# Kernel tuning notes

Hardware: AMD Instinct MI355X
Metric: run time of the kernel (lower is better)

The kernel has to match this reference:

```python
import jax, jax.numpy as jnp
import numpy as np
from jax import lax

H = 256        # hidden_size
T = 576        # history length (PERIOD*24)
F_T = 24       # future steps
M = 32         # m_features
B = 256        # batch
PERIOD = T // 24
E = 2 * H      # encoder output dim (bidirectional)
EPS = 1e-6     # torch PairwiseDistance eps


def setup_inputs() -> dict:
    key = jax.random.key(0)
    ks = jax.random.split(key, 16)
    rn = lambda k, sh, s=1.0: jax.random.normal(k, sh, jnp.float32) * s
    return {
        "input_encoded": rn(ks[0], (B, T, E)),
        "feature_history1": rn(ks[1], (B, T, M)),
        "y_history": rn(ks[2], (B, T, 1)),               # unused by forward (matches torch)
        "feature_future1": rn(ks[3], (B, F_T, M)),
        "hidden": rn(ks[4], (2, B, H), 0.1),
        "cell": rn(ks[5], (2, B, H), 0.1),
        # attn_layer: Linear(2H+M -> T), Tanh, Linear(T -> T)
        "attn_W1": rn(ks[6], (T, E + M), 0.05), "attn_b1": jnp.zeros((T,), jnp.float32),
        "attn_W2": rn(ks[7], (T, T), 0.05),     "attn_b2": jnp.zeros((T,), jnp.float32),
        # bidirectional 1-layer LSTM, stacked over direction d in {fwd, bwd}
        "W_ih": rn(ks[8], (2, 4 * H, E + M), 0.05),
        "W_hh": rn(ks[9], (2, 4 * H, H), 0.05),
        "b_ih": jnp.zeros((2, 4 * H), jnp.float32),
        "b_hh": jnp.zeros((2, 4 * H), jnp.float32),
        # fc_final: Linear(2H -> H), ReLU, Linear(H -> 1)
        "fcf_W1": rn(ks[10], (H, E), 0.05), "fcf_b1": jnp.zeros((H,), jnp.float32),
        "fcf_W2": rn(ks[11], (1, H), 0.05), "fcf_b2": jnp.zeros((1,), jnp.float32),
    }


def reference(input_encoded, feature_history1, y_history, feature_future1,
              hidden, cell, attn_W1, attn_b1, attn_W2, attn_b2,
              W_ih, W_hh, b_ih, b_hh, fcf_W1, fcf_b1, fcf_W2, fcf_b2):
    b = input_encoded.shape[0]
    # --- period-similarity weights alpha (computed once) ---
    fh = feature_history1.reshape(b, PERIOD, 24, M)                 # [B,period,24,M]
    # pairwise L2 distance between future [B,24,1,M] and history hours [B,24,period,M]
    diff = feature_future1[:, :, None, :] - fh.transpose(0, 2, 1, 3)  # [B,24,period,M]
    dist = jnp.sqrt(jnp.sum((diff + EPS) ** 2, axis=-1))            # [B,24,period]
    dp = 1.0 / jnp.sum(dist, axis=2)                                # rsqrt(.)**2 == 1/x; [B,24]
    alpha = jax.nn.softmax(dp, axis=1)                              # [B,24] (period==24)
    enc = input_encoded.reshape(b, PERIOD, 24, E)                   # [B,period,24,E]
    bias = (b_ih + b_hh)[:, None, :]                                # [2,1,4H]

    def step(carry, ff_t):                                          # ff_t: [B,M]
        h, c = carry                                                # each [2,B,H]
        x = jnp.concatenate([h[0], h[1], ff_t], axis=1)             # [B,2H+M]
        a = jnp.tanh(x @ attn_W1.T + attn_b1) @ attn_W2.T + attn_b2
        a = jax.nn.softmax(a, axis=1)                               # [B,T]
        w = a.reshape(b, PERIOD, 24)                                # [B,period,24]
        # context: sum attention-weighted encodings over each day, then alpha over periods
        ctx = jnp.einsum('bpk,bpke,bp->be', w, enc, alpha)          # [B,E]
        inp = jnp.concatenate([ctx, ff_t], axis=1)                  # [B,2H+M]
        gates = (jnp.einsum('bi,dgi->dbg', inp, W_ih)
                 + jnp.einsum('dbh,dgh->dbg', h, W_hh) + bias)      # [2,B,4H]
        i_g, f_g, g_g, o_g = jnp.split(gates, 4, axis=-1)           # torch gate order i,f,g,o
        c_new = jax.nn.sigmoid(f_g) * c + jax.nn.sigmoid(i_g) * jnp.tanh(g_g)
        h_new = jax.nn.sigmoid(o_g) * jnp.tanh(c_new)               # [2,B,H]
        hh = jnp.concatenate([h_new[0], h_new[1]], axis=1)          # [B,2H]
        y = jax.nn.relu(hh @ fcf_W1.T + fcf_b1) @ fcf_W2.T + fcf_b2  # [B,1]
        return (h_new, c_new), y

    _, ys = lax.scan(step, (hidden, cell), jnp.transpose(feature_future1, (1, 0, 2)))
    return jnp.transpose(ys, (1, 0, 2))                             # [B,f_T,1]
```

## Files before the change

kernel.cpp:

```cpp
#include <hip/hip_runtime.h>
#include <math.h>

#define B_ 256
#define T_ 576
#define FT_ 24
#define M_ 32
#define H_ 256
#define E_ 512
#define KX_ 544
#define ND_ 2048
#define EPS_ 1e-6f
#define LDAS 72

typedef __attribute__((ext_vector_type(8))) short bf8;
typedef __attribute__((ext_vector_type(4))) float f4;

__device__ __forceinline__ float bf2f(unsigned short s) {
    union { unsigned u; float f; } c; c.u = ((unsigned)s) << 16; return c.f;
}
__device__ __forceinline__ short f2bf(float f) {
    union { float f; unsigned u; } c; c.f = f;
    unsigned r = c.u + 0x7fffu + ((c.u >> 16) & 1u);
    return (short)(r >> 16);
}
__device__ __forceinline__ float sigm(float x) { return 1.f / (1.f + expf(-x)); }

__device__ __forceinline__ void mfma4(const short (*As)[LDAS], const short (*Bs)[LDAS],
                                      int wm, int wn, int fr, int fk, f4 acc[2][2]) {
    bf8 a0 = *(const bf8*)&As[wm + fr][fk];
    bf8 a1 = *(const bf8*)&As[wm + 16 + fr][fk];
    bf8 b0 = *(const bf8*)&Bs[wn + fr][fk];
    bf8 b1 = *(const bf8*)&Bs[wn + 16 + fr][fk];
    acc[0][0] = __builtin_amdgcn_mfma_f32_16x16x32_bf16(a0, b0, acc[0][0], 0, 0, 0);
    acc[0][1] = __builtin_amdgcn_mfma_f32_16x16x32_bf16(a0, b1, acc[0][1], 0, 0, 0);
    acc[1][0] = __builtin_amdgcn_mfma_f32_16x16x32_bf16(a1, b0, acc[1][0], 0, 0, 0);
    acc[1][1] = __builtin_amdgcn_mfma_f32_16x16x32_bf16(a1, b1, acc[1][1], 0, 0, 0);
}

__device__ __forceinline__ void gemm64(const short* __restrict__ A, int lda,
                                       const short* __restrict__ Wt, int ldw, int K,
                                       short (*As)[LDAS], short (*Bs)[LDAS], int tid,
                                       f4 acc[2][2]) {
    int lane = tid & 63, w = tid >> 6;
    int wm = (w & 1) * 32, wn = (w >> 1) * 32;
    int fr = lane & 15, fk = (lane >> 4) * 8;
    int r = tid >> 2, c0 = (tid & 3) * 16, c8 = (tid & 3) * 8;
    int4 pa0, pa1, pb0, pb1;
    auto ld = [&](int k0) {
        if (K - k0 >= 64) {
            pa0 = *(const int4*)(A + r * lda + k0 + c0);
            pa1 = *(const int4*)(A + r * lda + k0 + c0 + 8);
            pb0 = *(const int4*)(Wt + r * ldw + k0 + c0);
            pb1 = *(const int4*)(Wt + r * ldw + k0 + c0 + 8);
        } else {
            pa0 = *(const int4*)(A + r * lda + k0 + c8);
            pb0 = *(const int4*)(Wt + r * ldw + k0 + c8);
        }
    };
    ld(0);
    for (int k0 = 0; k0 < K; k0 += 64) {
        int rem = K - k0;
        if (rem >= 64) {
            *(int4*)&As[r][c0] = pa0; *(int4*)&As[r][c0 + 8] = pa1;
            *(int4*)&Bs[r][c0] = pb0; *(int4*)&Bs[r][c0 + 8] = pb1;
        } else {
            *(int4*)&As[r][c8] = pa0;
            *(int4*)&Bs[r][c8] = pb0;
        }
        __syncthreads();
        if (k0 + 64 < K) ld(k0 + 64);
        mfma4(As, Bs, wm, wn, fr, fk, acc);
        if (rem >= 64) mfma4(As, Bs, wm, wn, fr, fk + 32, acc);
        __syncthreads();
    }
}

struct SetupPrm {
    const float *enc, *fhist, *ff, *hidden, *cell;
    const float *aW1, *aW2, *Wih, *Whh, *bih, *bhh, *fW1;
    short *W1b, *W2b, *Wihb, *Whhb, *fW1b, *encb, *xb, *hA;
    float *bcomb, *alpha, *cbuf;
};

__global__ __launch_bounds__(256) void k_setup(SetupPrm p) {
    const int NT = 2048 * 256;
    int gt = blockIdx.x * 256 + threadIdx.x;
    auto cast = [&](const float* s, short* d, int n4) {
        for (int i = gt; i < n4; i += NT) {
            float4 v = ((const float4*)s)[i];
            short4 o; o.x = f2bf(v.x); o.y = f2bf(v.y); o.z = f2bf(v.z); o.w = f2bf(v.w);
            ((short4*)d)[i] = o;
        }
    };
    cast(p.aW1, p.W1b, T_ * KX_ / 4);
    cast(p.aW2, p.W2b, T_ * T_ / 4);
    cast(p.fW1, p.fW1b, H_ * E_ / 4);
    cast(p.enc, p.encb, B_ * T_ * E_ / 4);
    for (int i = gt; i < ND_ * KX_ / 4; i += NT) {
        int row = i / (KX_ / 4), c4 = i % (KX_ / 4);
        int d = row >> 10, rest = row & 1023, j = rest >> 2, g = rest & 3;
        int orig = d * 1024 + g * 256 + j;
        float4 v = ((const float4*)(p.Wih + orig * KX_))[c4];
        short4 o; o.x = f2bf(v.x); o.y = f2bf(v.y); o.z = f2bf(v.z); o.w = f2bf(v.w);
        ((short4*)(p.Wihb + row * KX_))[c4] = o;
    }
    for (int i = gt; i < ND_ * H_ / 4; i += NT) {
        int row = i / (H_ / 4), c4 = i % (H_ / 4);
        int d = row >> 10, rest = row & 1023, j = rest >> 2, g = rest & 3;
        int orig = d * 1024 + g * 256 + j;
        float4 v = ((const float4*)(p.Whh + orig * H_))[c4];
        short4 o; o.x = f2bf(v.x); o.y = f2bf(v.y); o.z = f2bf(v.z); o.w = f2bf(v.w);
        ((short4*)(p.Whhb + row * H_))[c4] = o;
    }
    for (int i = gt; i < ND_; i += NT) {
        int d = i >> 10, rest = i & 1023, j = rest >> 2, g = rest & 3;
        int orig = d * 1024 + g * 256 + j;
        p.bcomb[i] = p.bih[orig] + p.bhh[orig];
    }
    for (int i = gt; i < 2 * B_ * H_; i += NT) {
        int d = i >> 16, b = (i >> 8) & 255, j = i & 255;
        short hv = f2bf(p.hidden[i]);
        p.xb[b * KX_ + d * H_ + j] = hv;
        p.hA[i] = hv;
        p.cbuf[i] = p.cell[i];
        if (d == 0 && j < M_) p.xb[b * KX_ + E_ + j] = f2bf(p.ff[b * FT_ * M_ + j]);
    }
    if (blockIdx.x < 256 && threadIdx.x < 64) {
        int b = blockIdx.x, t = threadIdx.x;
        float dp = 0.f;
        if (t < 24) {
            float fv[M_];
            const float* fp = p.ff + (b * FT_ + t) * M_;
            #pragma unroll
            for (int m = 0; m < M_; m++) fv[m] = fp[m];
            float dist = 0.f;
            for (int pp = 0; pp < 24; pp++) {
                const float* hp = p.fhist + (b * T_ + pp * 24 + t) * M_;
                float s = 0.f;
                #pragma unroll
                for (int m = 0; m < M_; m++) { float d = fv[m] - hp[m] + EPS_; s += d * d; }
                dist += sqrtf(s);
            }
            dp = 1.f / dist;
        }
        float v = (t < 24) ? dp : -INFINITY;
        float mx = v;
        for (int off = 32; off; off >>= 1) mx = fmaxf(mx, __shfl_xor(mx, off));
        float e = (t < 24) ? expf(dp - mx) : 0.f;
        float sme = e;
        for (int off = 32; off; off >>= 1) sme += __shfl_xor(sme, off);
        if (t < 24) p.alpha[b * 24 + t] = e / sme;
    }
}

__global__ __launch_bounds__(256) void k_a1fc(const short* __restrict__ xb,
                                              const short* __restrict__ W1b,
                                              const float* __restrict__ ab1,
                                              short* __restrict__ s1,
                                              const short* __restrict__ fW1b,
                                              const float* __restrict__ fb1,
                                              const float* __restrict__ fW2,
                                              float* __restrict__ out, int t) {
    __shared__ short As[64][LDAS];
    __shared__ short Bs[64][LDAS];
    __shared__ float ypart[64];
    int tid = threadIdx.x;
    int lane = tid & 63, w = tid >> 6;
    int wm = (w & 1) * 32, wn = (w >> 1) * 32;
    int m0 = blockIdx.y * 64;
    if (blockIdx.x < 9) {
        int n0 = blockIdx.x * 64;
        f4 acc[2][2] = {};
        gemm64(xb + m0 * KX_, KX_, W1b + n0 * KX_, KX_, KX_, As, Bs, tid, acc);
        int colb = n0 + wn + (lane & 15);
        int rowb = m0 + wm + (lane >> 4) * 4;
        #pragma unroll
        for (int im = 0; im < 2; im++)
            #pragma unroll
            for (int in = 0; in < 2; in++) {
                int col = colb + in * 16;
                float bv = ab1[col];
                #pragma unroll
                for (int q = 0; q < 4; q++)
                    s1[(rowb + im * 16 + q) * T_ + col] = f2bf(tanhf(acc[im][in][q] + bv));
            }
    } else {
        if (t == 0) return;
        int step = t - 1;
        int n0 = (blockIdx.x - 9) * 64;
        f4 acc[2][2] = {};
        gemm64(xb + m0 * KX_, KX_, fW1b + n0 * E_, E_, E_, As, Bs, tid, acc);
        if (tid < 64) ypart[tid] = 0.f;
        __syncthreads();
        int colb = n0 + wn + (lane & 15);
        int rloc = wm + (lane >> 4) * 4;
        #pragma unroll
        for (int im = 0; im < 2; im++)
            #pragma unroll
            for (int q = 0; q < 4; q++) {
                float s = 0.f;
                #pragma unroll
                for (int in = 0; in < 2; in++) {
                    int col = colb + in * 16;
                    s += fmaxf(acc[im][in][q] + fb1[col], 0.f) * fW2[col];
                }
                #pragma unroll
                for (int off = 1; off < 16; off <<= 1) s += __shfl_xor(s, off);
                if ((lane & 15) == 0) atomicAdd(&ypart[rloc + im * 16 + q], s);
            }
        __syncthreads();
        if (tid < 64) atomicAdd(&out[(m0 + tid) * FT_ + step], ypart[tid]);
    }
}

__global__ __launch_bounds__(256) void k_a2(const short* __restrict__ s1,
                                            const short* __restrict__ W2b,
                                            const float* __restrict__ ab2,
                                            float* __restrict__ logit) {
    __shared__ short As[64][LDAS];
    __shared__ short Bs[64][LDAS];
    int n0 = blockIdx.x * 64, m0 = blockIdx.y * 64, tid = threadIdx.x;
    f4 acc[2][2] = {};
    gemm64(s1 + m0 * T_, T_, W2b + n0 * T_, T_, T_, As, Bs, tid, acc);
    int lane = tid & 63, w = tid >> 6;
    int wm = (w & 1) * 32, wn = (w >> 1) * 32;
    int colb = n0 + wn + (lane & 15);
    int rowb = m0 + wm + (lane >> 4) * 4;
    #pragma unroll
    for (int im = 0; im < 2; im++)
        #pragma unroll
        for (int in = 0; in < 2; in++) {
            int col = colb + in * 16;
            float bv = ab2[col];
            #pragma unroll
            for (int q = 0; q < 4; q++)
                logit[(rowb + im * 16 + q) * T_ + col] = acc[im][in][q] + bv;
        }
}

__global__ __launch_bounds__(256) void k_ctx(const float* __restrict__ logits,
                                             const float* __restrict__ alpha,
                                             const short* __restrict__ encb,
                                             float* __restrict__ ctx) {
    int b = blockIdx.x >> 3, s = blockIdx.x & 7;
    int tid = threadIdx.x;
    __shared__ float wt[T_];
    __shared__ float red4[4];
    __shared__ float red[8][64];
    const float* lg = logits + b * T_;
    float l0 = lg[tid], l1 = lg[tid + 256];
    float l2 = (tid < 64) ? lg[tid + 512] : -INFINITY;
    float mx = fmaxf(fmaxf(l0, l1), l2);
    for (int off = 32; off; off >>= 1) mx = fmaxf(mx, __shfl_xor(mx, off));
    if ((tid & 63) == 0) red4[tid >> 6] = mx;
    __syncthreads();
    mx = fmaxf(fmaxf(red4[0], red4[1]), fmaxf(red4[2], red4[3]));
    float e0 = expf(l0 - mx), e1 = expf(l1 - mx);
    float e2 = (tid < 64) ? expf(l2 - mx) : 0.f;
    float sme = e0 + e1 + e2;
    for (int off = 32; off; off >>= 1) sme += __shfl_xor(sme, off);
    __syncthreads();
    if ((tid & 63) == 0) red4[tid >> 6] = sme;
    __syncthreads();
    float inv = 1.f / (red4[0] + red4[1] + red4[2] + red4[3]);
    const float* al = alpha + b * 24;
    wt[tid]       = e0 * inv * al[tid / 24];
    wt[tid + 256] = e1 * inv * al[(tid + 256) / 24];
    if (tid < 64) wt[tid + 512] = e2 * inv * al[(tid + 512) / 24];
    __syncthreads();
    int chp = tid & 31, rg = tid >> 5;
    int c0 = s * 64;
    float a0 = 0.f, a1 = 0.f;
    const unsigned* ep = (const unsigned*)(encb + ((size_t)b * T_ + rg * 72) * E_ + c0) + chp;
    const float* wl = wt + rg * 72;
    #pragma unroll 8
    for (int it = 0; it < 72; it++) {
        float wv = wl[it];
        unsigned u = ep[(size_t)it * (E_ / 2)];
        a0 += wv * bf2f((unsigned short)(u & 0xffffu));
        a1 += wv * bf2f((unsigned short)(u >> 16));
    }
    *(float2*)&red[rg][chp * 2] = make_float2(a0, a1);
    __syncthreads();
    if (tid < 64) {
        float sum = 0.f;
        #pragma unroll
        for (int r = 0; r < 8; r++) sum += red[r][tid];
        ctx[b * E_ + c0 + tid] = sum;
    }
}

__global__ __launch_bounds__(256) void k_gl(const float* __restrict__ ctxp,
                                            const float* __restrict__ ff, int t,
                                            short* __restrict__ xb,
                                            const short* __restrict__ Wihb,
                                            const short* __restrict__ Whhb,
                                            const float* __restrict__ bcomb,
                                            float* __restrict__ cbuf,
                                            const short* __restrict__ hprev,
                                            short* __restrict__ hnext,
                                            const float* __restrict__ fb2,
                                            float* __restrict__ out) {
    __shared__ union {
        struct { short As[64][LDAS]; short Bs[64][LDAS]; } g;
        float gt[64][68];
    } sm;
    int n0 = blockIdx.x * 64, m0 = blockIdx.y * 64, tid = threadIdx.x;
    int lane = tid & 63, w = tid >> 6;
    int wm = (w & 1) * 32, wn = (w >> 1) * 32;
    int fr = lane & 15, fk = (lane >> 4) * 8;
    int r = tid >> 2, c0 = (tid & 3) * 16, c8 = (tid & 3) * 8;
    f4 acc[2][2] = {};
    for (int k0 = 0; k0 < KX_; k0 += 64) {
        int rem = KX_ - k0;
        if (rem >= 64) {
            const float* cp = ctxp + (m0 + r) * E_ + k0 + c0;
            short av[16];
            #pragma unroll
            for (int i = 0; i < 16; i++) av[i] = f2bf(cp[i]);
            *(int4*)&sm.g.As[r][c0]     = *(int4*)&av[0];
            *(int4*)&sm.g.As[r][c0 + 8] = *(int4*)&av[8];
            *(int4*)&sm.g.Bs[r][c0]     = *(const int4*)(Wihb + (n0 + r) * KX_ + k0 + c0);
            *(int4*)&sm.g.Bs[r][c0 + 8] = *(const int4*)(Wihb + (n0 + r) * KX_ + k0 + c0 + 8);
        } else {
            const float* fp = ff + ((m0 + r) * FT_ + t) * M_ + (k0 + c8 - E_);
            short av[8];
            #pragma unroll
            for (int i = 0; i < 8; i++) av[i] = f2bf(fp[i]);
            *(int4*)&sm.g.As[r][c8] = *(int4*)&av[0];
            *(int4*)&sm.g.Bs[r][c8] = *(const int4*)(Wihb + (n0 + r) * KX_ + k0 + c8);
        }
        __syncthreads();
        mfma4(sm.g.As, sm.g.Bs, wm, wn, fr, fk, acc);
        if (rem >= 64) mfma4(sm.g.As, sm.g.Bs, wm, wn, fr, fk + 32, acc);
        __syncthreads();
    }
    int d = n0 >> 10;
    gemm64(hprev + d * B_ * H_ + m0 * H_, H_, Whhb + n0 * H_, H_, H_,
           sm.g.As, sm.g.Bs, tid, acc);
    int clb = wn + (lane & 15);
    int rlb = wm + (lane >> 4) * 4;
    #pragma unroll
    for (int im = 0; im < 2; im++)
        #pragma unroll
        for (int in = 0; in < 2; in++) {
            int cl = clb + in * 16;
            float bv = bcomb[n0 + cl];
            #pragma unroll
            for (int q = 0; q < 4; q++)
                sm.gt[rlb + im * 16 + q][cl] = acc[im][in][q] + bv;
        }
    __syncthreads();
    int j0 = (n0 >> 2) & 255;
    #pragma unroll
    for (int it = 0; it < 4; it++) {
        int item = tid + it * 256;
        int rl = item >> 4, ql = item & 15;
        float ig = sm.gt[rl][ql * 4 + 0];
        float fg = sm.gt[rl][ql * 4 + 1];
        float gg = sm.gt[rl][ql * 4 + 2];
        float og = sm.gt[rl][ql * 4 + 3];
        int b = m0 + rl, j = j0 + ql;
        int ci = d * 65536 + b * 256 + j;
        float cn = sigm(fg) * cbuf[ci] + sigm(ig) * tanhf(gg);
        float hn = sigm(og) * tanhf(cn);
        cbuf[ci] = cn;
        short hv = f2bf(hn);
        xb[b * KX_ + d * H_ + j] = hv;
        hnext[ci] = hv;
        if (d == 0 && j < M_ && t + 1 < FT_)
            xb[b * KX_ + E_ + j] = f2bf(ff[(b * FT_ + t + 1) * M_ + j]);
        if (n0 == 0 && ql == 0) out[b * FT_ + t] = fb2[0];
    }
}

__global__ __launch_bounds__(256) void k_fc(const short* __restrict__ xb,
                                            const short* __restrict__ fW1b,
                                            const float* __restrict__ fb1,
                                            const float* __restrict__ fW2,
                                            float* __restrict__ out, int step) {
    __shared__ short As[64][LDAS];
    __shared__ short Bs[64][LDAS];
    __shared__ float ypart[64];
    int fb = blockIdx.x, tid = threadIdx.x;
    int m0 = (fb >> 2) * 64, n0 = (fb & 3) * 64;
    f4 acc[2][2] = {};
    gemm64(xb + m0 * KX_, KX_, fW1b + n0 * E_, E_, E_, As, Bs, tid, acc);
    if (tid < 64) ypart[tid] = 0.f;
    __syncthreads();
    int lane = tid & 63, w = tid >> 6;
    int wm = (w & 1) * 32, wn = (w >> 1) * 32;
    int colb = n0 + wn + (lane & 15);
    int rloc = wm + (lane >> 4) * 4;
    #pragma unroll
    for (int im = 0; im < 2; im++)
        #pragma unroll
        for (int q = 0; q < 4; q++) {
            float s = 0.f;
            #pragma unroll
            for (int in = 0; in < 2; in++) {
                int col = colb + in * 16;
                s += fmaxf(acc[im][in][q] + fb1[col], 0.f) * fW2[col];
            }
            #pragma unroll
            for (int off = 1; off < 16; off <<= 1) s += __shfl_xor(s, off);
            if ((lane & 15) == 0) atomicAdd(&ypart[rloc + im * 16 + q], s);
        }
    __syncthreads();
    if (tid < 64) atomicAdd(&out[(m0 + tid) * FT_ + step], ypart[tid]);
}

extern "C" void kernel_launch(void* const* d_in, const int* in_sizes, int n_in,
                              void* d_out, int out_size, void* d_ws, size_t ws_size,
                              hipStream_t stream) {
    (void)in_sizes; (void)n_in; (void)out_size; (void)ws_size;
    const float* enc_f  = (const float*)d_in[0];
    const float* fhist  = (const float*)d_in[1];
    const float* ff     = (const float*)d_in[3];
    const float* hidden = (const float*)d_in[4];
    const float* cell   = (const float*)d_in[5];
    const float* aW1    = (const float*)d_in[6];
    const float* ab1    = (const float*)d_in[7];
    const float* aW2    = (const float*)d_in[8];
    const float* ab2    = (const float*)d_in[9];
    const float* Wih    = (const float*)d_in[10];
    const float* Whh    = (const float*)d_in[11];
    const float* bih    = (const float*)d_in[12];
    const float* bhh    = (const float*)d_in[13];
    const float* fW1    = (const float*)d_in[14];
    const float* fb1    = (const float*)d_in[15];
    const float* fW2    = (const float*)d_in[16];
    const float* fb2    = (const float*)d_in[17];
    float* out = (float*)d_out;

    char* pws = (char*)d_ws;
    auto take = [&](size_t n) { char* r = pws; pws += (n + 255) & ~(size_t)255; return r; };
    float* alpha = (float*)take(B_ * 24 * 4);
    short* xb    = (short*)take(B_ * KX_ * 2);
    short* hA    = (short*)take(2 * B_ * H_ * 2);
    short* hB    = (short*)take(2 * B_ * H_ * 2);
    float* cbuf  = (float*)take(2 * B_ * H_ * 4);
    short* s1    = (short*)take(B_ * T_ * 2);
    float* logit = (float*)take(B_ * T_ * 4);
    float* ctxp  = (float*)take(B_ * E_ * 4);
    float* bcomb = (float*)take(ND_ * 4);
    short* W1b   = (short*)take(T_ * KX_ * 2);
    short* W2b   = (short*)take(T_ * T_ * 2);
    short* Wihb  = (short*)take(ND_ * KX_ * 2);
    short* Whhb  = (short*)take(ND_ * H_ * 2);
    short* fW1b  = (short*)take(H_ * E_ * 2);
    short* encb  = (short*)take((size_t)B_ * T_ * E_ * 2);

    SetupPrm sp;
    sp.enc = enc_f; sp.fhist = fhist; sp.ff = ff; sp.hidden = hidden; sp.cell = cell;
    sp.aW1 = aW1; sp.aW2 = aW2; sp.Wih = Wih; sp.Whh = Whh; sp.bih = bih; sp.bhh = bhh;
    sp.fW1 = fW1;
    sp.W1b = W1b; sp.W2b = W2b; sp.Wihb = Wihb; sp.Whhb = Whhb; sp.fW1b = fW1b;
    sp.encb = encb; sp.xb = xb; sp.hA = hA;
    sp.bcomb = bcomb; sp.alpha = alpha; sp.cbuf = cbuf;

    k_setup<<<2048, 256, 0, stream>>>(sp);

    for (int t = 0; t < FT_; t++) {
        k_a1fc<<<dim3(13, 4), 256, 0, stream>>>(xb, W1b, ab1, s1, fW1b, fb1, fW2, out, t);
        k_a2<<<dim3(9, 4), 256, 0, stream>>>(s1, W2b, ab2, logit);
        k_ctx<<<B_ * 8, 256, 0, stream>>>(logit, alpha, encb, ctxp);
        const short* hprev = (t & 1) ? hB : hA;
        short* hnext       = (t & 1) ? hA : hB;
        k_gl<<<dim3(ND_ / 64, B_ / 64), 256, 0, stream>>>(ctxp, ff, t, xb, Wihb, Whhb,
                                                          bcomb, cbuf, hprev, hnext, fb2, out);
    }
    k_fc<<<16, 256, 0, stream>>>(xb, fW1b, fb1, fW2, out, FT_ - 1);
}
```

Measured before the change: 1.858 ms.

## Fuse per-step kernels into one persistent kernel with grid barriers

Replaces the 24×4 kernel launches of the decoder loop with a single persistent kernel of 256 blocks that runs all stages and separates them with a software grid-wide barrier built on atomics. The context stage is remapped from 8 blocks per batch row to one block per batch row, each reading a full 576×512 encoding slab with 16-byte loads. The aim is to remove launch overhead and inter-kernel gaps. In exchange, most blocks sit idle during the small GEMM stages, and the barrier relies on all 256 blocks being co-resident on the device.

```diff
diff --git a/kernel.cpp b/kernel.cpp
--- a/kernel.cpp
+++ b/kernel.cpp
@@ -11,6 +11,7 @@
 #define ND_ 2048
 #define EPS_ 1e-6f
 #define LDAS 72
+#define NBLK 256
 
 typedef __attribute__((ext_vector_type(8))) short bf8;
 typedef __attribute__((ext_vector_type(4))) float f4;
@@ -24,6 +25,24 @@
     return (short)(r >> 16);
 }
 __device__ __forceinline__ float sigm(float x) { return 1.f / (1.f + expf(-x)); }
+
+__device__ __forceinline__ void gbar(unsigned* bar) {
+    __syncthreads();
+    if (threadIdx.x == 0) {
+        __threadfence();
+        unsigned gen = __hip_atomic_load(&bar[1], __ATOMIC_RELAXED, __HIP_MEMORY_SCOPE_AGENT);
+        unsigned a = __hip_atomic_fetch_add(&bar[0], 1u, __ATOMIC_ACQ_REL, __HIP_MEMORY_SCOPE_AGENT);
+        if (a == NBLK - 1u) {
+            __hip_atomic_store(&bar[0], 0u, __ATOMIC_RELAXED, __HIP_MEMORY_SCOPE_AGENT);
+            __hip_atomic_fetch_add(&bar[1], 1u, __ATOMIC_RELEASE, __HIP_MEMORY_SCOPE_AGENT);
+        } else {
+            while (__hip_atomic_load(&bar[1], __ATOMIC_ACQUIRE, __HIP_MEMORY_SCOPE_AGENT) == gen)
+                __builtin_amdgcn_s_sleep(2);
+        }
+        __threadfence();
+    }
+    __syncthreads();
+}
 
 __device__ __forceinline__ void mfma4(const short (*As)[LDAS], const short (*Bs)[LDAS],
                                       int wm, int wn, int fr, int fk, f4 acc[2][2]) {
@@ -80,11 +99,13 @@
     const float *aW1, *aW2, *Wih, *Whh, *bih, *bhh, *fW1;
     short *W1b, *W2b, *Wihb, *Whhb, *fW1b, *encb, *xb, *hA;
     float *bcomb, *alpha, *cbuf;
+    unsigned *bar;
 };
 
 __global__ __launch_bounds__(256) void k_setup(SetupPrm p) {
     const int NT = 2048 * 256;
     int gt = blockIdx.x * 256 + threadIdx.x;
+    if (gt == 0) { p.bar[0] = 0; p.bar[1] = 0; }
     auto cast = [&](const float* s, short* d, int n4) {
         for (int i = gt; i < n4; i += NT) {
             float4 v = ((const float4*)s)[i];
@@ -153,239 +174,23 @@
     }
 }
 
-__global__ __launch_bounds__(256) void k_a1fc(const short* __restrict__ xb,
-                                              const short* __restrict__ W1b,
-                                              const float* __restrict__ ab1,
-                                              short* __restrict__ s1,
-                                              const short* __restrict__ fW1b,
-                                              const float* __restrict__ fb1,
-                                              const float* __restrict__ fW2,
-                                              float* __restrict__ out, int t) {
-    __shared__ short As[64][LDAS];
-    __shared__ short Bs[64][LDAS];
-    __shared__ float ypart[64];
-    int tid = threadIdx.x;
-    int lane = tid & 63, w = tid >> 6;
-    int wm = (w & 1) * 32, wn = (w >> 1) * 32;
-    int m0 = blockIdx.y * 64;
-    if (blockIdx.x < 9) {
-        int n0 = blockIdx.x * 64;
-        f4 acc[2][2] = {};
-        gemm64(xb + m0 * KX_, KX_, W1b + n0 * KX_, KX_, KX_, As, Bs, tid, acc);
-        int colb = n0 + wn + (lane & 15);
-        int rowb = m0 + wm + (lane >> 4) * 4;
-        #pragma unroll
-        for (int im = 0; im < 2; im++)
-            #pragma unroll
-            for (int in = 0; in < 2; in++) {
-                int col = colb + in * 16;
-                float bv = ab1[col];
-                #pragma unroll
-                for (int q = 0; q < 4; q++)
-                    s1[(rowb + im * 16 + q) * T_ + col] = f2bf(tanhf(acc[im][in][q] + bv));
-            }
-    } else {
-        if (t == 0) return;
-        int step = t - 1;
-        int n0 = (blockIdx.x - 9) * 64;
-        f4 acc[2][2] = {};
-        gemm64(xb + m0 * KX_, KX_, fW1b + n0 * E_, E_, E_, As, Bs, tid, acc);
-        if (tid < 64) ypart[tid] = 0.f;
-        __syncthreads();
-        int colb = n0 + wn + (lane & 15);
-        int rloc = wm + (lane >> 4) * 4;
-        #pragma unroll
-        for (int im = 0; im < 2; im++)
-            #pragma unroll
-            for (int q = 0; q < 4; q++) {
-                float s = 0.f;
-                #pragma unroll
-                for (int in = 0; in < 2; in++) {
-                    int col = colb + in * 16;
-                    s += fmaxf(acc[im][in][q] + fb1[col], 0.f) * fW2[col];
-                }
-                #pragma unroll
-                for (int off = 1; off < 16; off <<= 1) s += __shfl_xor(s, off);
-                if ((lane & 15) == 0) atomicAdd(&ypart[rloc + im * 16 + q], s);
-            }
-        __syncthreads();
-        if (tid < 64) atomicAdd(&out[(m0 + tid) * FT_ + step], ypart[tid]);
-    }
-}
-
-__global__ __launch_bounds__(256) void k_a2(const short* __restrict__ s1,
-                                            const short* __restrict__ W2b,
-                                            const float* __restrict__ ab2,
-                                            float* __restrict__ logit) {
-    __shared__ short As[64][LDAS];
-    __shared__ short Bs[64][LDAS];
-    int n0 = blockIdx.x * 64, m0 = blockIdx.y * 64, tid = threadIdx.x;
+struct LoopPrm {
+    short *xb;
+    const short *W1b, *W2b, *Wihb, *Whhb, *fW1b, *encb;
+    const float *ab1, *ab2, *fb1, *fW2, *fb2, *ff;
+    const float *bcomb, *alpha;
+    short *s1;
+    float *logit, *ctxp, *cbuf;
+    short *hA, *hB;
+    float *out;
+    unsigned *bar;
+};
+
+__device__ __forceinline__ void fc_tile(const LoopPrm& p, int m0, int n0, int step,
+                                        short (*As)[LDAS], short (*Bs)[LDAS],
+                                        float* ypart, int tid) {
     f4 acc[2][2] = {};
-    gemm64(s1 + m0 * T_, T_, W2b + n0 * T_, T_, T_, As, Bs, tid, acc);
-    int lane = tid & 63, w = tid >> 6;
-    int wm = (w & 1) * 32, wn = (w >> 1) * 32;
-    int colb = n0 + wn + (lane & 15);
-    int rowb = m0 + wm + (lane >> 4) * 4;
-    #pragma unroll
-    for (int im = 0; im < 2; im++)
-        #pragma unroll
-        for (int in = 0; in < 2; in++) {
-            int col = colb + in * 16;
-            float bv = ab2[col];
-            #pragma unroll
-            for (int q = 0; q < 4; q++)
-                logit[(rowb + im * 16 + q) * T_ + col] = acc[im][in][q] + bv;
-        }
-}
-
-__global__ __launch_bounds__(256) void k_ctx(const float* __restrict__ logits,
-                                             const float* __restrict__ alpha,
-                                             const short* __restrict__ encb,
-                                             float* __restrict__ ctx) {
-    int b = blockIdx.x >> 3, s = blockIdx.x & 7;
-    int tid = threadIdx.x;
-    __shared__ float wt[T_];
-    __shared__ float red4[4];
-    __shared__ float red[8][64];
-    const float* lg = logits + b * T_;
-    float l0 = lg[tid], l1 = lg[tid + 256];
-    float l2 = (tid < 64) ? lg[tid + 512] : -INFINITY;
-    float mx = fmaxf(fmaxf(l0, l1), l2);
-    for (int off = 32; off; off >>= 1) mx = fmaxf(mx, __shfl_xor(mx, off));
-    if ((tid & 63) == 0) red4[tid >> 6] = mx;
-    __syncthreads();
-    mx = fmaxf(fmaxf(red4[0], red4[1]), fmaxf(red4[2], red4[3]));
-    float e0 = expf(l0 - mx), e1 = expf(l1 - mx);
-    float e2 = (tid < 64) ? expf(l2 - mx) : 0.f;
-    float sme = e0 + e1 + e2;
-    for (int off = 32; off; off >>= 1) sme += __shfl_xor(sme, off);
-    __syncthreads();
-    if ((tid & 63) == 0) red4[tid >> 6] = sme;
-    __syncthreads();
-    float inv = 1.f / (red4[0] + red4[1] + red4[2] + red4[3]);
-    const float* al = alpha + b * 24;
-    wt[tid]       = e0 * inv * al[tid / 24];
-    wt[tid + 256] = e1 * inv * al[(tid + 256) / 24];
-    if (tid < 64) wt[tid + 512] = e2 * inv * al[(tid + 512) / 24];
-    __syncthreads();
-    int chp = tid & 31, rg = tid >> 5;
-    int c0 = s * 64;
-    float a0 = 0.f, a1 = 0.f;
-    const unsigned* ep = (const unsigned*)(encb + ((size_t)b * T_ + rg * 72) * E_ + c0) + chp;
-    const float* wl = wt + rg * 72;
-    #pragma unroll 8
-    for (int it = 0; it < 72; it++) {
-        float wv = wl[it];
-        unsigned u = ep[(size_t)it * (E_ / 2)];
-        a0 += wv * bf2f((unsigned short)(u & 0xffffu));
-        a1 += wv * bf2f((unsigned short)(u >> 16));
-    }
-    *(float2*)&red[rg][chp * 2] = make_float2(a0, a1);
-    __syncthreads();
-    if (tid < 64) {
-        float sum = 0.f;
-        #pragma unroll
-        for (int r = 0; r < 8; r++) sum += red[r][tid];
-        ctx[b * E_ + c0 + tid] = sum;
-    }
-}
-
-__global__ __launch_bounds__(256) void k_gl(const float* __restrict__ ctxp,
-                                            const float* __restrict__ ff, int t,
-                                            short* __restrict__ xb,
-                                            const short* __restrict__ Wihb,
-                                            const short* __restrict__ Whhb,
-                                            const float* __restrict__ bcomb,
-                                            float* __restrict__ cbuf,
-                                            const short* __restrict__ hprev,
-                                            short* __restrict__ hnext,
-                                            const float* __restrict__ fb2,
-                                            float* __restrict__ out) {
-    __shared__ union {
-        struct { short As[64][LDAS]; short Bs[64][LDAS]; } g;
-        float gt[64][68];
-    } sm;
-    int n0 = blockIdx.x * 64, m0 = blockIdx.y * 64, tid = threadIdx.x;
-    int lane = tid & 63, w = tid >> 6;
-    int wm = (w & 1) * 32, wn = (w >> 1) * 32;
-    int fr = lane & 15, fk = (lane >> 4) * 8;
-    int r = tid >> 2, c0 = (tid & 3) * 16, c8 = (tid & 3) * 8;
-    f4 acc[2][2] = {};
-    for (int k0 = 0; k0 < KX_; k0 += 64) {
-        int rem = KX_ - k0;
-        if (rem >= 64) {
-            const float* cp = ctxp + (m0 + r) * E_ + k0 + c0;
-            short av[16];
-            #pragma unroll
-            for (int i = 0; i < 16; i++) av[i] = f2bf(cp[i]);
-            *(int4*)&sm.g.As[r][c0]     = *(int4*)&av[0];
-            *(int4*)&sm.g.As[r][c0 + 8] = *(int4*)&av[8];
-            *(int4*)&sm.g.Bs[r][c0]     = *(const int4*)(Wihb + (n0 + r) * KX_ + k0 + c0);
-            *(int4*)&sm.g.Bs[r][c0 + 8] = *(const int4*)(Wihb + (n0 + r) * KX_ + k0 + c0 + 8);
-        } else {
-            const float* fp = ff + ((m0 + r) * FT_ + t) * M_ + (k0 + c8 - E_);
-            short av[8];
-            #pragma unroll
-            for (int i = 0; i < 8; i++) av[i] = f2bf(fp[i]);
-            *(int4*)&sm.g.As[r][c8] = *(int4*)&av[0];
-            *(int4*)&sm.g.Bs[r][c8] = *(const int4*)(Wihb + (n0 + r) * KX_ + k0 + c8);
-        }
-        __syncthreads();
-        mfma4(sm.g.As, sm.g.Bs, wm, wn, fr, fk, acc);
-        if (rem >= 64) mfma4(sm.g.As, sm.g.Bs, wm, wn, fr, fk + 32, acc);
-        __syncthreads();
-    }
-    int d = n0 >> 10;
-    gemm64(hprev + d * B_ * H_ + m0 * H_, H_, Whhb + n0 * H_, H_, H_,
-           sm.g.As, sm.g.Bs, tid, acc);
-    int clb = wn + (lane & 15);
-    int rlb = wm + (lane >> 4) * 4;
-    #pragma unroll
-    for (int im = 0; im < 2; im++)
-        #pragma unroll
-        for (int in = 0; in < 2; in++) {
-            int cl = clb + in * 16;
-            float bv = bcomb[n0 + cl];
-            #pragma unroll
-            for (int q = 0; q < 4; q++)
-                sm.gt[rlb + im * 16 + q][cl] = acc[im][in][q] + bv;
-        }
-    __syncthreads();
-    int j0 = (n0 >> 2) & 255;
-    #pragma unroll
-    for (int it = 0; it < 4; it++) {
-        int item = tid + it * 256;
-        int rl = item >> 4, ql = item & 15;
-        float ig = sm.gt[rl][ql * 4 + 0];
-        float fg = sm.gt[rl][ql * 4 + 1];
-        float gg = sm.gt[rl][ql * 4 + 2];
-        float og = sm.gt[rl][ql * 4 + 3];
-        int b = m0 + rl, j = j0 + ql;
-        int ci = d * 65536 + b * 256 + j;
-        float cn = sigm(fg) * cbuf[ci] + sigm(ig) * tanhf(gg);
-        float hn = sigm(og) * tanhf(cn);
-        cbuf[ci] = cn;
-        short hv = f2bf(hn);
-        xb[b * KX_ + d * H_ + j] = hv;
-        hnext[ci] = hv;
-        if (d == 0 && j < M_ && t + 1 < FT_)
-            xb[b * KX_ + E_ + j] = f2bf(ff[(b * FT_ + t + 1) * M_ + j]);
-        if (n0 == 0 && ql == 0) out[b * FT_ + t] = fb2[0];
-    }
-}
-
-__global__ __launch_bounds__(256) void k_fc(const short* __restrict__ xb,
-                                            const short* __restrict__ fW1b,
-                                            const float* __restrict__ fb1,
-                                            const float* __restrict__ fW2,
-                                            float* __restrict__ out, int step) {
-    __shared__ short As[64][LDAS];
-    __shared__ short Bs[64][LDAS];
-    __shared__ float ypart[64];
-    int fb = blockIdx.x, tid = threadIdx.x;
-    int m0 = (fb >> 2) * 64, n0 = (fb & 3) * 64;
-    f4 acc[2][2] = {};
-    gemm64(xb + m0 * KX_, KX_, fW1b + n0 * E_, E_, E_, As, Bs, tid, acc);
+    gemm64(p.xb + m0 * KX_, KX_, p.fW1b + n0 * E_, E_, E_, As, Bs, tid, acc);
     if (tid < 64) ypart[tid] = 0.f;
     __syncthreads();
     int lane = tid & 63, w = tid >> 6;
@@ -400,14 +205,202 @@
             #pragma unroll
             for (int in = 0; in < 2; in++) {
                 int col = colb + in * 16;
-                s += fmaxf(acc[im][in][q] + fb1[col], 0.f) * fW2[col];
+                s += fmaxf(acc[im][in][q] + p.fb1[col], 0.f) * p.fW2[col];
             }
             #pragma unroll
             for (int off = 1; off < 16; off <<= 1) s += __shfl_xor(s, off);
             if ((lane & 15) == 0) atomicAdd(&ypart[rloc + im * 16 + q], s);
         }
     __syncthreads();
-    if (tid < 64) atomicAdd(&out[(m0 + tid) * FT_ + step], ypart[tid]);
+    if (tid < 64) atomicAdd(&p.out[(m0 + tid) * FT_ + step], ypart[tid]);
+}
+
+__global__ __launch_bounds__(256) void k_loop(LoopPrm p) {
+    __shared__ union {
+        struct { short As[64][LDAS]; short Bs[64][LDAS]; float ypart[64]; } g;
+        struct { float wt[T_]; float red4[4]; float red[4][512]; } c;
+        float gt[64][68];
+    } sm;
+    const int blk = blockIdx.x, tid = threadIdx.x;
+    const int lane = tid & 63, w = tid >> 6;
+    const int wm = (w & 1) * 32, wn = (w >> 1) * 32;
+
+    for (int t = 0; t < FT_; t++) {
+        if (blk < 36) {
+            int m0 = (blk / 9) * 64, n0 = (blk % 9) * 64;
+            f4 acc[2][2] = {};
+            gemm64(p.xb + m0 * KX_, KX_, p.W1b + n0 * KX_, KX_, KX_,
+                   sm.g.As, sm.g.Bs, tid, acc);
+            int colb = n0 + wn + (lane & 15);
+            int rowb = m0 + wm + (lane >> 4) * 4;
+            #pragma unroll
+            for (int im = 0; im < 2; im++)
+                #pragma unroll
+                for (int in = 0; in < 2; in++) {
+                    int col = colb + in * 16;
+                    float bv = p.ab1[col];
+                    #pragma unroll
+                    for (int q = 0; q < 4; q++)
+                        p.s1[(rowb + im * 16 + q) * T_ + col] =
+                            f2bf(tanhf(acc[im][in][q] + bv));
+                }
+        } else if (blk < 52 && t > 0) {
+            int u = blk - 36;
+            fc_tile(p, (u >> 2) * 64, (u & 3) * 64, t - 1,
+                    sm.g.As, sm.g.Bs, sm.g.ypart, tid);
+        }
+        gbar(p.bar);
+
+        if (blk < 36) {
+            int m0 = (blk / 9) * 64, n0 = (blk % 9) * 64;
+            f4 acc[2][2] = {};
+            gemm64(p.s1 + m0 * T_, T_, p.W2b + n0 * T_, T_, T_,
+                   sm.g.As, sm.g.Bs, tid, acc);
+            int colb = n0 + wn + (lane & 15);
+            int rowb = m0 + wm + (lane >> 4) * 4;
+            #pragma unroll
+            for (int im = 0; im < 2; im++)
+                #pragma unroll
+                for (int in = 0; in < 2; in++) {
+                    int col = colb + in * 16;
+                    float bv = p.ab2[col];
+                    #pragma unroll
+                    for (int q = 0; q < 4; q++)
+                        p.logit[(rowb + im * 16 + q) * T_ + col] = acc[im][in][q] + bv;
+                }
+        }
+        gbar(p.bar);
+
+        {
+            int b = blk;
+            const float* lg = p.logit + b * T_;
+            float l0 = lg[tid], l1 = lg[tid + 256];
+            float l2 = (tid < 64) ? lg[tid + 512] : -INFINITY;
+            float mx = fmaxf(fmaxf(l0, l1), l2);
+            for (int off = 32; off; off >>= 1) mx = fmaxf(mx, __shfl_xor(mx, off));
+            if (lane == 0) sm.c.red4[w] = mx;
+            __syncthreads();
+            mx = fmaxf(fmaxf(sm.c.red4[0], sm.c.red4[1]),
+                       fmaxf(sm.c.red4[2], sm.c.red4[3]));
+            float e0 = expf(l0 - mx), e1 = expf(l1 - mx);
+            float e2 = (tid < 64) ? expf(l2 - mx) : 0.f;
+            float sme = e0 + e1 + e2;
+            for (int off = 32; off; off >>= 1) sme += __shfl_xor(sme, off);
+            __syncthreads();
+            if (lane == 0) sm.c.red4[w] = sme;
+            __syncthreads();
+            float inv = 1.f / (sm.c.red4[0] + sm.c.red4[1] + sm.c.red4[2] + sm.c.red4[3]);
+            const float* al = p.alpha + b * 24;
+            sm.c.wt[tid]       = e0 * inv * al[tid / 24];
+            sm.c.wt[tid + 256] = e1 * inv * al[(tid + 256) / 24];
+            if (tid < 64) sm.c.wt[tid + 512] = e2 * inv * al[(tid + 512) / 24];
+            __syncthreads();
+            int oct = tid & 63, rp = tid >> 6;
+            const short* ebase = p.encb + (size_t)b * T_ * E_ + oct * 8;
+            float a0 = 0.f, a1 = 0.f, a2 = 0.f, a3 = 0.f;
+            float a4 = 0.f, a5 = 0.f, a6 = 0.f, a7 = 0.f;
+            #pragma unroll 4
+            for (int r = rp; r < T_; r += 4) {
+                float wv = sm.c.wt[r];
+                int4 v = *(const int4*)(ebase + (size_t)r * E_);
+                a0 += wv * bf2f((unsigned short)v.x);
+                a1 += wv * bf2f((unsigned short)(((unsigned)v.x) >> 16));
+                a2 += wv * bf2f((unsigned short)v.y);
+                a3 += wv * bf2f((unsigned short)(((unsigned)v.y) >> 16));
+                a4 += wv * bf2f((unsigned short)v.z);
+                a5 += wv * bf2f((unsigned short)(((unsigned)v.z) >> 16));
+                a6 += wv * bf2f((unsigned short)v.w);
+                a7 += wv * bf2f((unsigned short)(((unsigned)v.w) >> 16));
+            }
+            float* rr = &sm.c.red[rp][oct * 8];
+            rr[0] = a0; rr[1] = a1; rr[2] = a2; rr[3] = a3;
+            rr[4] = a4; rr[5] = a5; rr[6] = a6; rr[7] = a7;
+            __syncthreads();
+            float s0 = 0.f, s1v = 0.f;
+            #pragma unroll
+            for (int q = 0; q < 4; q++) {
+                s0  += sm.c.red[q][tid * 2];
+                s1v += sm.c.red[q][tid * 2 + 1];
+            }
+            p.ctxp[b * E_ + tid * 2]     = s0;
+            p.ctxp[b * E_ + tid * 2 + 1] = s1v;
+        }
+        gbar(p.bar);
+
+        if (blk < 128) {
+            int n0 = (blk & 31) * 64, m0 = (blk >> 5) * 64;
+            int fr = lane & 15, fk = (lane >> 4) * 8;
+            int r = tid >> 2, c0 = (tid & 3) * 16, c8 = (tid & 3) * 8;
+            f4 acc[2][2] = {};
+            for (int k0 = 0; k0 < KX_; k0 += 64) {
+                int rem = KX_ - k0;
+                if (rem >= 64) {
+                    const float* cp = p.ctxp + (m0 + r) * E_ + k0 + c0;
+                    short av[16];
+                    #pragma unroll
+                    for (int i = 0; i < 16; i++) av[i] = f2bf(cp[i]);
+                    *(int4*)&sm.g.As[r][c0]     = *(int4*)&av[0];
+                    *(int4*)&sm.g.As[r][c0 + 8] = *(int4*)&av[8];
+                    *(int4*)&sm.g.Bs[r][c0]     = *(const int4*)(p.Wihb + (n0 + r) * KX_ + k0 + c0);
+                    *(int4*)&sm.g.Bs[r][c0 + 8] = *(const int4*)(p.Wihb + (n0 + r) * KX_ + k0 + c0 + 8);
+                } else {
+                    const float* fp = p.ff + ((m0 + r) * FT_ + t) * M_ + (k0 + c8 - E_);
+                    short av[8];
+                    #pragma unroll
+                    for (int i = 0; i < 8; i++) av[i] = f2bf(fp[i]);
+                    *(int4*)&sm.g.As[r][c8] = *(int4*)&av[0];
+                    *(int4*)&sm.g.Bs[r][c8] = *(const int4*)(p.Wihb + (n0 + r) * KX_ + k0 + c8);
+                }
+                __syncthreads();
+                mfma4(sm.g.As, sm.g.Bs, wm, wn, fr, fk, acc);
+                if (rem >= 64) mfma4(sm.g.As, sm.g.Bs, wm, wn, fr, fk + 32, acc);
+                __syncthreads();
+            }
+            int d = n0 >> 10;
+            const short* hprev = (t & 1) ? p.hB : p.hA;
+            short* hnext       = (t & 1) ? p.hA : p.hB;
+            gemm64(hprev + d * B_ * H_ + m0 * H_, H_, p.Whhb + n0 * H_, H_, H_,
+                   sm.g.As, sm.g.Bs, tid, acc);
+            int clb = wn + (lane & 15);
+            int rlb = wm + (lane >> 4) * 4;
+            #pragma unroll
+            for (int im = 0; im < 2; im++)
+                #pragma unroll
+                for (int in = 0; in < 2; in++) {
+                    int cl = clb + in * 16;
+                    float bv = p.bcomb[n0 + cl];
+                    #pragma unroll
+                    for (int q = 0; q < 4; q++)
+                        sm.gt[rlb + im * 16 + q][cl] = acc[im][in][q] + bv;
+                }
+            __syncthreads();
+            int j0 = (n0 >> 2) & 255;
+            #pragma unroll
+            for (int it = 0; it < 4; it++) {
+                int item = tid + it * 256;
+                int rl = item >> 4, ql = item & 15;
+                float ig = sm.gt[rl][ql * 4 + 0];
+                float fg = sm.gt[rl][ql * 4 + 1];
+                float gg = sm.gt[rl][ql * 4 + 2];
+                float og = sm.gt[rl][ql * 4 + 3];
+                int b = m0 + rl, j = j0 + ql;
+                int ci = d * 65536 + b * 256 + j;
+                float cn = sigm(fg) * p.cbuf[ci] + sigm(ig) * tanhf(gg);
+                float hn = sigm(og) * tanhf(cn);
+                p.cbuf[ci] = cn;
+                short hv = f2bf(hn);
+                p.xb[b * KX_ + d * H_ + j] = hv;
+                hnext[ci] = hv;
+                if (d == 0 && j < M_ && t + 1 < FT_)
+                    p.xb[b * KX_ + E_ + j] = f2bf(p.ff[(b * FT_ + t + 1) * M_ + j]);
+                if (n0 == 0 && ql == 0) p.out[b * FT_ + t] = p.fb2[0];
+            }
+        }
+        gbar(p.bar);
+    }
+    if (blk < 16)
+        fc_tile(p, (blk >> 2) * 64, (blk & 3) * 64, FT_ - 1,
+                sm.g.As, sm.g.Bs, sm.g.ypart, tid);
 }
 
 extern "C" void kernel_launch(void* const* d_in, const int* in_sizes, int n_in,
@@ -435,6 +428,7 @@
 
     char* pws = (char*)d_ws;
     auto take = [&](size_t n) { char* r = pws; pws += (n + 255) & ~(size_t)255; return r; };
+    unsigned* bar = (unsigned*)take(256);
     float* alpha = (float*)take(B_ * 24 * 4);
     short* xb    = (short*)take(B_ * KX_ * 2);
     short* hA    = (short*)take(2 * B_ * H_ * 2);
@@ -458,17 +452,20 @@
     sp.W1b = W1b; sp.W2b = W2b; sp.Wihb = Wihb; sp.Whhb = Whhb; sp.fW1b = fW1b;
     sp.encb = encb; sp.xb = xb; sp.hA = hA;
     sp.bcomb = bcomb; sp.alpha = alpha; sp.cbuf = cbuf;
+    sp.bar = bar;
 
     k_setup<<<2048, 256, 0, stream>>>(sp);
 
-    for (int t = 0; t < FT_; t++) {
-        k_a1fc<<<dim3(13, 4), 256, 0, stream>>>(xb, W1b, ab1, s1, fW1b, fb1, fW2, out, t);
-        k_a2<<<dim3(9, 4), 256, 0, stream>>>(s1, W2b, ab2, logit);
-        k_ctx<<<B_ * 8, 256, 0, stream>>>(logit, alpha, encb, ctxp);
-        const short* hprev = (t & 1) ? hB : hA;
-        short* hnext       = (t & 1) ? hA : hB;
-        k_gl<<<dim3(ND_ / 64, B_ / 64), 256, 0, stream>>>(ctxp, ff, t, xb, Wihb, Whhb,
-                                                          bcomb, cbuf, hprev, hnext, fb2, out);
-    }
-    k_fc<<<16, 256, 0, stream>>>(xb, fW1b, fb1, fW2, out, FT_ - 1);
-}
+    LoopPrm lp;
+    lp.xb = xb;
+    lp.W1b = W1b; lp.W2b = W2b; lp.Wihb = Wihb; lp.Whhb = Whhb; lp.fW1b = fW1b;
+    lp.encb = encb;
+    lp.ab1 = ab1; lp.ab2 = ab2; lp.fb1 = fb1; lp.fW2 = fW2; lp.fb2 = fb2; lp.ff = ff;
+    lp.bcomb = bcomb; lp.alpha = alpha;
+    lp.s1 = s1; lp.logit = logit; lp.ctxp = ctxp; lp.cbuf = cbuf;
+    lp.hA = hA; lp.hB = hB;
+    lp.out = out;
+    lp.bar = bar;
+
+    k_loop<<<NBLK, 256, 0, stream>>>(lp);
+}
```

Result: slower. 6.157 ms (+231.4%).
